# Optimization experiments

Hardware: AMD Instinct MI355X
Metric: run time of the kernel (lower is better)

## Reference

```python
import jax, jax.numpy as jnp
import numpy as np

B, L, NB = 8192, 40, 2        # batch, maxlen, behavior features
V, E = 100000, 64             # vocab per table, embed dim per table
NS, ND = 3, 8                 # other sparse feats, dense feats
D = NB * E                    # concatenated behavior embed dim = 128
ALL = D + D + (ND + NS * E)   # info_all dim = 456
NEG_INF = -2.0**32 + 1
BN_EPS = 1e-3                 # keras BatchNormalization default epsilon


def setup_inputs() -> dict:
    key = jax.random.key(0)
    ks = jax.random.split(key, 20)
    inp = {
        "dense_inputs": jax.random.normal(ks[0], (B, ND), jnp.float32),
        "sparse_inputs": jax.random.randint(ks[1], (B, NS), 0, V),
        "seq_inputs": jax.random.randint(ks[2], (B, L, NB), 0, V),
        "item_inputs": jax.random.randint(ks[3], (B, NB), 0, V),
        # embedding tables (random_uniform init in keras)
        "emb_sparse": jax.random.uniform(ks[4], (NS, V, E), jnp.float32, -0.05, 0.05),
        "emb_seq": jax.random.uniform(ks[5], (NB, V, E), jnp.float32, -0.05, 0.05),
        # attention MLP: input 4*D=512 -> 80 -> 40 -> 1
        "att_W1": jax.random.normal(ks[6], (4 * D, 80), jnp.float32) * 0.05,
        "att_b1": jnp.zeros((80,), jnp.float32),
        "att_W2": jax.random.normal(ks[7], (80, 40), jnp.float32) * 0.05,
        "att_b2": jnp.zeros((40,), jnp.float32),
        "att_Wf": jax.random.normal(ks[8], (40, 1), jnp.float32) * 0.05,
        "att_bf": jnp.zeros((1,), jnp.float32),
        # batch norm (inference-mode moving stats)
        "bn_gamma": jnp.ones((ALL,), jnp.float32),
        "bn_beta": jnp.zeros((ALL,), jnp.float32),
        "bn_mean": jnp.zeros((ALL,), jnp.float32),
        "bn_var": jnp.ones((ALL,), jnp.float32),
        # FFN: ALL -> 80 -> 40 -> 1, PReLU alphas per-feature
        "ffn_W1": jax.random.normal(ks[9], (ALL, 80), jnp.float32) * 0.05,
        "ffn_b1": jnp.zeros((80,), jnp.float32),
        "ffn_a1": jnp.full((80,), 0.25, jnp.float32),
        "ffn_W2": jax.random.normal(ks[10], (80, 40), jnp.float32) * 0.05,
        "ffn_b2": jnp.zeros((40,), jnp.float32),
        "ffn_a2": jnp.full((40,), 0.25, jnp.float32),
        "out_W": jax.random.normal(ks[11], (40, 1), jnp.float32) * 0.05,
        "out_b": jnp.zeros((1,), jnp.float32),
    }
    return inp


def prelu(x, alpha):
    return jnp.where(x > 0, x, alpha * x)


def reference(dense_inputs, sparse_inputs, seq_inputs, item_inputs,
              emb_sparse, emb_seq,
              att_W1, att_b1, att_W2, att_b2, att_Wf, att_bf,
              bn_gamma, bn_beta, bn_mean, bn_var,
              ffn_W1, ffn_b1, ffn_a1, ffn_W2, ffn_b2, ffn_a2,
              out_W, out_b):
    mask = (seq_inputs[:, :, 0] != 0)                                   # [B, L]
    # other sparse embeddings + dense features
    other_info = jnp.concatenate(
        [dense_inputs] + [emb_sparse[i][sparse_inputs[:, i]] for i in range(NS)], axis=-1)
    # behavior sequence / candidate item embeddings
    seq_embed = jnp.concatenate([emb_seq[i][seq_inputs[:, :, i]] for i in range(NB)], axis=-1)  # [B,L,D]
    item_embed = jnp.concatenate([emb_seq[i][item_inputs[:, i]] for i in range(NB)], axis=-1)   # [B,D]

    # local activation attention
    q = jnp.broadcast_to(item_embed[:, None, :], seq_embed.shape)       # [B,L,D]
    info = jnp.concatenate([q, seq_embed, q - seq_embed, q * seq_embed], axis=-1)  # [B,L,4D]
    h = jax.nn.sigmoid(info @ att_W1 + att_b1)
    h = jax.nn.sigmoid(h @ att_W2 + att_b2)
    logits = (h @ att_Wf + att_bf)[..., 0]                               # [B,L]
    logits = jnp.where(mask, logits, NEG_INF)
    att = jax.nn.softmax(logits, axis=-1)                                # [B,L]
    user_info = jnp.einsum('bl,bld->bd', att, seq_embed)                 # [B,D]

    info_all = jnp.concatenate([user_info, item_embed, other_info], axis=-1)  # [B,ALL]
    info_all = bn_gamma * (info_all - bn_mean) * jax.lax.rsqrt(bn_var + BN_EPS) + bn_beta
    info_all = prelu(info_all @ ffn_W1 + ffn_b1, ffn_a1)
    info_all = prelu(info_all @ ffn_W2 + ffn_b2, ffn_a2)
    return jax.nn.sigmoid(info_all @ out_W + out_b)                      # [B,1]
```

## Files before the change

### kernel.cpp

```cpp
#include <hip/hip_runtime.h>

#define BB 8192
#define LL 40
#define VV 100000
#define NEG_INF_F (-4294967295.0f)
#define XS 264
#define HS 104
#define XGS 480

typedef __attribute__((ext_vector_type(8))) short short8;
typedef __attribute__((ext_vector_type(4))) float f32x4;

__device__ __forceinline__ unsigned short f2bf(float f) {
  unsigned u = __float_as_uint(f);
  u += 0x7FFFu + ((u >> 16) & 1u);
  return (unsigned short)(u >> 16);
}
__device__ __forceinline__ float bf2f(unsigned short s) {
  return __uint_as_float(((unsigned)s) << 16);
}

__global__ void prep_all(const float* __restrict__ W1, float* __restrict__ wqcT,
                         unsigned short* __restrict__ WsdpT,
                         const float* __restrict__ aW2, unsigned short* __restrict__ W2bT,
                         const float* __restrict__ fW2, unsigned short* __restrict__ W2fT,
                         const float* __restrict__ fW1, const float* __restrict__ g,
                         const float* __restrict__ vr, unsigned short* __restrict__ W1fT,
                         const float* __restrict__ fb1, const float* __restrict__ be,
                         const float* __restrict__ mn, float* __restrict__ b1p) {
  __shared__ float red[4];
  int bid = blockIdx.x, t = threadIdx.x;
  if (bid < 40) {
    int i = bid * 256 + t;
    int h = i >> 7, k = i & 127;
    float a = W1[k * 80 + h];
    float b = W1[(128 + k) * 80 + h];
    float c = W1[(256 + k) * 80 + h];
    float d = W1[(384 + k) * 80 + h];
    wqcT[h * 132 + k] = a + c;
    WsdpT[h * 256 + k] = f2bf(b - c);
    WsdpT[h * 256 + 128 + k] = f2bf(d);
  } else if (bid < 58) {
    int i = (bid - 40) * 256 + t;
    int n = i / 96, k = i % 96;
    W2bT[i] = (n < 40 && k < 80) ? f2bf(aW2[k * 40 + n]) : (unsigned short)0;
  } else if (bid < 76) {
    int i = (bid - 58) * 256 + t;
    int n = i / 96, k = i % 96;
    W2fT[i] = (n < 40 && k < 80) ? f2bf(fW2[k * 40 + n]) : (unsigned short)0;
  } else if (bid < 226) {
    int i = (bid - 76) * 256 + t;
    int n = i / 480, k = i % 480;
    float v = 0.f;
    if (k < 456) v = fW1[k * 80 + n] * g[k] * rsqrtf(vr[k] + 1e-3f);
    W1fT[i] = f2bf(v);
  } else {
    int n = bid - 226;
    float p = 0.f;
    for (int k = t; k < 456; k += 256) {
      float sc = g[k] * rsqrtf(vr[k] + 1e-3f);
      p += (be[k] - mn[k] * sc) * fW1[k * 80 + n];
    }
    for (int off = 32; off; off >>= 1) p += __shfl_xor(p, off, 64);
    if ((t & 63) == 0) red[t >> 6] = p;
    __syncthreads();
    if (t == 0) b1p[n] = fb1[n] + red[0] + red[1] + red[2] + red[3];
  }
}


__launch_bounds__(256, 5)
__global__ void din_att(const float* __restrict__ dense, const int* __restrict__ sparsei,
                        const int* __restrict__ seqi, const int* __restrict__ itemi,
                        const float* __restrict__ embS, const float* __restrict__ embQ,
                        const float* __restrict__ wqcT, const unsigned short* __restrict__ WsdpT,
                        const unsigned short* __restrict__ W2bT,
                        const float* __restrict__ ab1, const float* __restrict__ ab2,
                        const float* __restrict__ aWf, const float* __restrict__ abf,
                        unsigned short* __restrict__ Xg) {
  __shared__ __align__(16) char smem[31392];
  unsigned short* sX  = (unsigned short*)smem;
  unsigned short* sH1 = (unsigned short*)smem + 10560;
  float* sQ     = (float*)(smem + 29440);
  float* sQC    = sQ + 128;
  float* sOther = sQC + 80;
  float* sAtt   = sOther + 200;
  float* sLogit = sAtt + 40;

  const int t = threadIdx.x;
  const int b = blockIdx.x;
  const int wv = t >> 6, ln = t & 63, m16 = ln & 15, quad = ln >> 4;

  short8 Bf[8];
  {
    const unsigned short* br = WsdpT + (size_t)(wv * 16 + m16) * 256 + quad * 8;
#pragma unroll
    for (int kt = 0; kt < 8; kt++) Bf[kt] = *(const short8*)(br + kt * 32);
  }

  if (t < 32) {
    int f = t >> 4, sub = t & 15;
    int idx = itemi[b * 2 + f];
    float4 v = *(const float4*)(embQ + ((size_t)(f * VV + idx)) * 64 + sub * 4);
    *(float4*)(sQ + f * 64 + sub * 4) = v;
  } else if (t < 80) {
    int j = t - 32, f = j >> 4, sub = j & 15;
    int idx = sparsei[b * 3 + f];
    float4 v = *(const float4*)(embS + ((size_t)(f * VV + idx)) * 64 + sub * 4);
    *(float4*)(sOther + 8 + f * 64 + sub * 4) = v;
  } else if (t < 88) {
    sOther[t - 80] = dense[b * 8 + (t - 80)];
  } else if (t < 128) {
    sLogit[t - 88] = 0.f;
  }
  for (int i = t; i < 1280; i += 256) {
    int r = i >> 4, sub = i & 15;
    int l = r >> 1, f = r & 1;
    int idx = seqi[b * 80 + r];
    float4 v = *(const float4*)(embQ + ((size_t)(f * VV + idx)) * 64 + sub * 4);
    ushort4 u;
    u.x = f2bf(v.x); u.y = f2bf(v.y); u.z = f2bf(v.z); u.w = f2bf(v.w);
    *(ushort4*)(sX + l * XS + f * 64 + sub * 4) = u;
  }
  for (int i = t; i < 320; i += 256) {
    int r = i >> 3, c = i & 7;
    ((unsigned*)sH1)[r * 52 + 40 + c] = 0u;
  }
  __syncthreads();

  if (t < 80) {
    float acc = ab1[t];
    const float* wq = wqcT + t * 132;
    for (int k = 0; k < 128; k += 4) {
      float4 w = *(const float4*)(wq + k);
      float4 q = *(const float4*)(sQ + k);
      acc += q.x * w.x + q.y * w.y + q.z * w.z + q.w * w.w;
    }
    sQC[t] = acc;
  } else {
    for (int i = t - 80; i < 2560; i += 176) {
      int l = i >> 6, kp = i & 63;
      unsigned sv = *(const unsigned*)(sX + l * XS + 2 * kp);
      float s0 = bf2f((unsigned short)sv);
      float s1 = bf2f((unsigned short)(sv >> 16));
      float p0 = sQ[2 * kp] * s0, p1 = sQ[2 * kp + 1] * s1;
      *(unsigned*)(sX + l * XS + 128 + 2 * kp) =
          (unsigned)f2bf(p0) | ((unsigned)f2bf(p1) << 16);
    }
  }
  __syncthreads();

  {
    const int h = wv * 16 + m16;
    const float qc = sQC[h];
#pragma unroll
    for (int mt = 0; mt < 3; mt++) {
      f32x4 acc = {0.f, 0.f, 0.f, 0.f};
      const unsigned short* ar = sX + (mt * 16 + m16) * XS + quad * 8;
#pragma unroll
      for (int kt = 0; kt < 8; kt++) {
        short8 a = *(const short8*)(ar + kt * 32);
        acc = __builtin_amdgcn_mfma_f32_16x16x32_bf16(a, Bf[kt], acc, 0, 0, 0);
      }
#pragma unroll
      for (int r = 0; r < 4; r++) {
        int l = mt * 16 + quad * 4 + r;
        if (l < 40) {
          float z = acc[r] + qc;
          sH1[l * HS + h] = f2bf(1.f / (1.f + __expf(-z)));
        }
      }
    }
    if (wv < 3) {
      short8 B4[8];
      const unsigned short* br = WsdpT + (size_t)(64 + m16) * 256 + quad * 8;
#pragma unroll
      for (int kt = 0; kt < 8; kt++) B4[kt] = *(const short8*)(br + kt * 32);
      f32x4 acc = {0.f, 0.f, 0.f, 0.f};
      const unsigned short* ar = sX + (wv * 16 + m16) * XS + quad * 8;
#pragma unroll
      for (int kt = 0; kt < 8; kt++) {
        short8 a = *(const short8*)(ar + kt * 32);
        acc = __builtin_amdgcn_mfma_f32_16x16x32_bf16(a, B4[kt], acc, 0, 0, 0);
      }
      int h4 = 64 + m16;
      float qc4 = sQC[h4];
#pragma unroll
      for (int r = 0; r < 4; r++) {
        int l = wv * 16 + quad * 4 + r;
        if (l < 40) {
          float z = acc[r] + qc4;
          sH1[l * HS + h4] = f2bf(1.f / (1.f + __expf(-z)));
        }
      }
    }
  }
  __syncthreads();

  for (int tile = wv; tile < 9; tile += 4) {
    int mt = tile / 3, nt = tile % 3;
    f32x4 acc = {0.f, 0.f, 0.f, 0.f};
    const unsigned short* ar = sH1 + (mt * 16 + m16) * HS + quad * 8;
    const unsigned short* br = W2bT + (nt * 16 + m16) * 96 + quad * 8;
#pragma unroll
    for (int kt = 0; kt < 3; kt++) {
      short8 a = *(const short8*)(ar + kt * 32);
      short8 bb = *(const short8*)(br + kt * 32);
      acc = __builtin_amdgcn_mfma_f32_16x16x32_bf16(a, bb, acc, 0, 0, 0);
    }
    int j = nt * 16 + m16;
    float b2 = (j < 40) ? ab2[j] : 0.f;
    float wf = (j < 40) ? aWf[j] : 0.f;
    float c[4];
#pragma unroll
    for (int r = 0; r < 4; r++) {
      float h2 = 1.f / (1.f + __expf(-(acc[r] + b2)));
      c[r] = (j < 40) ? h2 * wf : 0.f;
    }
#pragma unroll
    for (int off = 1; off < 16; off <<= 1) {
#pragma unroll
      for (int r = 0; r < 4; r++) c[r] += __shfl_xor(c[r], off, 64);
    }
    if (m16 == 0) {
#pragma unroll
      for (int r = 0; r < 4; r++) {
        int l = mt * 16 + quad * 4 + r;
        if (l < 40) atomicAdd(&sLogit[l], c[r]);
      }
    }
  }
  __syncthreads();

  if (wv == 0) {
    float logit = -3.0e38f;
    if (t < 40) {
      logit = (seqi[b * 80 + 2 * t] != 0) ? (sLogit[t] + abf[0]) : NEG_INF_F;
    }
    float mx = logit;
    for (int off = 32; off; off >>= 1) mx = fmaxf(mx, __shfl_xor(mx, off, 64));
    float ex = (t < 40) ? __expf(logit - mx) : 0.f;
    float sm = ex;
    for (int off = 32; off; off >>= 1) sm += __shfl_xor(sm, off, 64);
    if (t < 40) sAtt[t] = ex / sm;
  } else {
    int j = t - 64;
    unsigned* xr = (unsigned*)(Xg + (size_t)b * XGS);
    if (j < 64) {
      xr[64 + j] = (unsigned)f2bf(sQ[2 * j]) | ((unsigned)f2bf(sQ[2 * j + 1]) << 16);
    } else if (j < 164) {
      int p = j - 64;
      xr[128 + p] = (unsigned)f2bf(sOther[2 * p]) | ((unsigned)f2bf(sOther[2 * p + 1]) << 16);
    } else if (j < 176) {
      xr[228 + (j - 164)] = 0u;
    }
  }
  __syncthreads();

  if (t < 128) {
    float acc = 0.f;
    for (int l = 0; l < 40; l++) acc += sAtt[l] * bf2f(sX[l * XS + t]);
    Xg[(size_t)b * XGS + t] = f2bf(acc);
  }
}


__launch_bounds__(256, 2)
__global__ void din_ffn(const unsigned short* __restrict__ Xg,
                        const unsigned short* __restrict__ W1fT, const float* __restrict__ b1p,
                        const float* __restrict__ fa1,
                        const unsigned short* __restrict__ W2fT, const float* __restrict__ fb2,
                        const float* __restrict__ fa2,
                        const float* __restrict__ oW, const float* __restrict__ ob,
                        float* __restrict__ out) {
  __shared__ __align__(16) unsigned short sXB[16 * 488];
  __shared__ __align__(16) unsigned short sH1B[16 * HS];
  __shared__ float sH2B[16 * 41];
  const int t = threadIdx.x, blk = blockIdx.x;
  const int wv = t >> 6, ln = t & 63, m16 = ln & 15, quad = ln >> 4;

  short8 Bf[15];
  {
    const unsigned short* br = W1fT + (size_t)(wv * 16 + m16) * 480 + quad * 8;
#pragma unroll
    for (int kt = 0; kt < 15; kt++) Bf[kt] = *(const short8*)(br + kt * 32);
  }

  for (int i = t; i < 960; i += 256) {
    int r = i / 60, c = i % 60;
    *(uint4*)(sXB + r * 488 + c * 8) =
        *(const uint4*)(Xg + (size_t)(blk * 16 + r) * XGS + c * 8);
  }
  if (t < 128) {
    int r = t >> 3, c = t & 7;
    ((unsigned*)sH1B)[r * 52 + 40 + c] = 0u;
  }
  __syncthreads();

  {
    int h = wv * 16 + m16;
    f32x4 acc = {0.f, 0.f, 0.f, 0.f};
    const unsigned short* ar = sXB + m16 * 488 + quad * 8;
#pragma unroll
    for (int kt = 0; kt < 15; kt++) {
      short8 a = *(const short8*)(ar + kt * 32);
      acc = __builtin_amdgcn_mfma_f32_16x16x32_bf16(a, Bf[kt], acc, 0, 0, 0);
    }
    float b1v = b1p[h], a1v = fa1[h];
#pragma unroll
    for (int r = 0; r < 4; r++) {
      int l = quad * 4 + r;
      float z = acc[r] + b1v;
      z = z > 0.f ? z : a1v * z;
      sH1B[l * HS + h] = f2bf(z);
    }
    if (wv == 0) {
      short8 B4[15];
      const unsigned short* br = W1fT + (size_t)(64 + m16) * 480 + quad * 8;
#pragma unroll
      for (int kt = 0; kt < 15; kt++) B4[kt] = *(const short8*)(br + kt * 32);
      f32x4 acc4 = {0.f, 0.f, 0.f, 0.f};
#pragma unroll
      for (int kt = 0; kt < 15; kt++) {
        short8 a = *(const short8*)(ar + kt * 32);
        acc4 = __builtin_amdgcn_mfma_f32_16x16x32_bf16(a, B4[kt], acc4, 0, 0, 0);
      }
      int h4 = 64 + m16;
      float b1v4 = b1p[h4], a1v4 = fa1[h4];
#pragma unroll
      for (int r = 0; r < 4; r++) {
        int l = quad * 4 + r;
        float z = acc4[r] + b1v4;
        z = z > 0.f ? z : a1v4 * z;
        sH1B[l * HS + h4] = f2bf(z);
      }
    }
  }
  __syncthreads();

  if (wv < 3) {
    f32x4 acc = {0.f, 0.f, 0.f, 0.f};
    const unsigned short* ar = sH1B + m16 * HS + quad * 8;
    const unsigned short* br = W2fT + (wv * 16 + m16) * 96 + quad * 8;
#pragma unroll
    for (int kt = 0; kt < 3; kt++) {
      short8 a = *(const short8*)(ar + kt * 32);
      short8 bb = *(const short8*)(br + kt * 32);
      acc = __builtin_amdgcn_mfma_f32_16x16x32_bf16(a, bb, acc, 0, 0, 0);
    }
    int j = wv * 16 + m16;
    if (j < 40) {
      float b2 = fb2[j], a2 = fa2[j];
#pragma unroll
      for (int r = 0; r < 4; r++) {
        int l = quad * 4 + r;
        float z = acc[r] + b2;
        sH2B[l * 41 + j] = z > 0.f ? z : a2 * z;
      }
    }
  }
  __syncthreads();

  if (t < 16) {
    float acc = ob[0];
    for (int j = 0; j < 40; j++) acc += sH2B[t * 41 + j] * oW[j];
    out[blk * 16 + t] = 1.f / (1.f + __expf(-acc));
  }
}


extern "C" void kernel_launch(void* const* d_in, const int* in_sizes, int n_in,
                              void* d_out, int out_size, void* d_ws, size_t ws_size,
                              hipStream_t stream) {
  const float* dense  = (const float*)d_in[0];
  const int*   sparsei = (const int*)d_in[1];
  const int*   seqi   = (const int*)d_in[2];
  const int*   itemi  = (const int*)d_in[3];
  const float* embS   = (const float*)d_in[4];
  const float* embQ   = (const float*)d_in[5];
  const float* aW1    = (const float*)d_in[6];
  const float* ab1    = (const float*)d_in[7];
  const float* aW2    = (const float*)d_in[8];
  const float* ab2    = (const float*)d_in[9];
  const float* aWf    = (const float*)d_in[10];
  const float* abf    = (const float*)d_in[11];
  const float* bng    = (const float*)d_in[12];
  const float* bnb    = (const float*)d_in[13];
  const float* bnm    = (const float*)d_in[14];
  const float* bnv    = (const float*)d_in[15];
  const float* fW1    = (const float*)d_in[16];
  const float* fb1    = (const float*)d_in[17];
  const float* fa1    = (const float*)d_in[18];
  const float* fW2    = (const float*)d_in[19];
  const float* fb2    = (const float*)d_in[20];
  const float* fa2    = (const float*)d_in[21];
  const float* oW     = (const float*)d_in[22];
  const float* ob     = (const float*)d_in[23];
  float* out = (float*)d_out;

  float* ws = (float*)d_ws;
  float* wqcT = ws;
  float* b1p  = ws + 10560;
  unsigned short* WsdpT = (unsigned short*)(ws + 10640);
  unsigned short* W2bT  = (unsigned short*)(ws + 20880);
  unsigned short* W2fT  = (unsigned short*)(ws + 23184);
  unsigned short* W1fT  = (unsigned short*)(ws + 25488);
  unsigned short* Xg    = (unsigned short*)(ws + 44688);

  prep_all<<<306, 256, 0, stream>>>(aW1, wqcT, WsdpT, aW2, W2bT, fW2, W2fT,
                                    fW1, bng, bnv, W1fT, fb1, bnb, bnm, b1p);
  din_att<<<BB, 256, 0, stream>>>(dense, sparsei, seqi, itemi, embS, embQ,
                                  wqcT, WsdpT, W2bT, ab1, ab2, aWf, abf, Xg);
  din_ffn<<<512, 256, 0, stream>>>(Xg, W1fT, b1p, fa1, W2fT, fb2, fa2, oW, ob, out);
}
```

Baseline: 328.1 us.

## Fold item-query product into per-block attention weights to halve MFMA K

The per-element q*seq product columns are no longer built in shared memory. Each block instead forms fused B fragments W_sd + q∘W_d in registers, so the first attention layer runs over K=128 instead of 256. This shrinks the sX tile and total LDS, which allows raising launch bounds to 6 blocks per SM. The query-constant dot product is split across 160 threads, and the sequence mask is precomputed during the gather instead of reread from global memory. The fused weights are rounded to bf16 per batch, which slightly changes numerics.

```diff
diff --git a/kernel.cpp b/kernel.cpp
--- a/kernel.cpp
+++ b/kernel.cpp
@@ -4,7 +4,7 @@
 #define LL 40
 #define VV 100000
 #define NEG_INF_F (-4294967295.0f)
-#define XS 264
+#define XS 136
 #define HS 104
 #define XGS 480
 
@@ -18,6 +18,15 @@
 }
 __device__ __forceinline__ float bf2f(unsigned short s) {
   return __uint_as_float(((unsigned)s) << 16);
+}
+
+__device__ __forceinline__ short8 fuseB(short8 wsd, short8 wd, float4 qa, float4 qb) {
+  float qv[8] = {qa.x, qa.y, qa.z, qa.w, qb.x, qb.y, qb.z, qb.w};
+  short8 o;
+#pragma unroll
+  for (int j = 0; j < 8; j++)
+    o[j] = (short)f2bf(bf2f((unsigned short)wsd[j]) + qv[j] * bf2f((unsigned short)wd[j]));
+  return o;
 }
 
 __global__ void prep_all(const float* __restrict__ W1, float* __restrict__ wqcT,
@@ -69,7 +78,7 @@
 }
 
 
-__launch_bounds__(256, 5)
+__launch_bounds__(256, 6)
 __global__ void din_att(const float* __restrict__ dense, const int* __restrict__ sparsei,
                         const int* __restrict__ seqi, const int* __restrict__ itemi,
                         const float* __restrict__ embS, const float* __restrict__ embQ,
@@ -78,24 +87,28 @@
                         const float* __restrict__ ab1, const float* __restrict__ ab2,
                         const float* __restrict__ aWf, const float* __restrict__ abf,
                         unsigned short* __restrict__ Xg) {
-  __shared__ __align__(16) char smem[31392];
+  __shared__ __align__(16) char smem[21632];
   unsigned short* sX  = (unsigned short*)smem;
-  unsigned short* sH1 = (unsigned short*)smem + 10560;
-  float* sQ     = (float*)(smem + 29440);
-  float* sQC    = sQ + 128;
-  float* sOther = sQC + 80;
+  unsigned short* sH1 = (unsigned short*)(smem + 10880);
+  float* sQ     = (float*)(smem + 19200);
+  float* sQCp   = sQ + 128;
+  float* sOther = sQCp + 160;
   float* sAtt   = sOther + 200;
   float* sLogit = sAtt + 40;
+  float* sMask  = sLogit + 40;
 
   const int t = threadIdx.x;
   const int b = blockIdx.x;
   const int wv = t >> 6, ln = t & 63, m16 = ln & 15, quad = ln >> 4;
 
-  short8 Bf[8];
+  short8 wsdF[4], wdF[4];
   {
     const unsigned short* br = WsdpT + (size_t)(wv * 16 + m16) * 256 + quad * 8;
 #pragma unroll
-    for (int kt = 0; kt < 8; kt++) Bf[kt] = *(const short8*)(br + kt * 32);
+    for (int kt = 0; kt < 4; kt++) {
+      wsdF[kt] = *(const short8*)(br + kt * 32);
+      wdF[kt]  = *(const short8*)(br + 128 + kt * 32);
+    }
   }
 
   if (t < 32) {
@@ -121,6 +134,7 @@
     ushort4 u;
     u.x = f2bf(v.x); u.y = f2bf(v.y); u.z = f2bf(v.z); u.w = f2bf(v.w);
     *(ushort4*)(sX + l * XS + f * 64 + sub * 4) = u;
+    if (((r & 1) | sub) == 0) sMask[l] = (idx != 0) ? 0.f : NEG_INF_F;
   }
   for (int i = t; i < 320; i += 256) {
     int r = i >> 3, c = i & 7;
@@ -128,39 +142,52 @@
   }
   __syncthreads();
 
-  if (t < 80) {
-    float acc = ab1[t];
-    const float* wq = wqcT + t * 132;
-    for (int k = 0; k < 128; k += 4) {
+  if (t < 160) {
+    int h = (t < 80) ? t : t - 80;
+    int k0 = (t < 80) ? 0 : 64;
+    float acc = (t < 80) ? ab1[h] : 0.f;
+    const float* wq = wqcT + h * 132 + k0;
+    const float* qq = sQ + k0;
+    for (int k = 0; k < 64; k += 4) {
       float4 w = *(const float4*)(wq + k);
-      float4 q = *(const float4*)(sQ + k);
+      float4 q = *(const float4*)(qq + k);
       acc += q.x * w.x + q.y * w.y + q.z * w.z + q.w * w.w;
     }
-    sQC[t] = acc;
-  } else {
-    for (int i = t - 80; i < 2560; i += 176) {
-      int l = i >> 6, kp = i & 63;
-      unsigned sv = *(const unsigned*)(sX + l * XS + 2 * kp);
-      float s0 = bf2f((unsigned short)sv);
-      float s1 = bf2f((unsigned short)(sv >> 16));
-      float p0 = sQ[2 * kp] * s0, p1 = sQ[2 * kp + 1] * s1;
-      *(unsigned*)(sX + l * XS + 128 + 2 * kp) =
-          (unsigned)f2bf(p0) | ((unsigned)f2bf(p1) << 16);
+    sQCp[t] = acc;
+  }
+  short8 Bp[4], Bp4[4];
+  {
+#pragma unroll
+    for (int kt = 0; kt < 4; kt++) {
+      int k0 = quad * 8 + kt * 32;
+      float4 qa = *(const float4*)(sQ + k0);
+      float4 qb = *(const float4*)(sQ + k0 + 4);
+      Bp[kt] = fuseB(wsdF[kt], wdF[kt], qa, qb);
+    }
+    if (wv < 3) {
+      const unsigned short* br = WsdpT + (size_t)(64 + m16) * 256 + quad * 8;
+#pragma unroll
+      for (int kt = 0; kt < 4; kt++) {
+        short8 w1 = *(const short8*)(br + kt * 32);
+        short8 w2 = *(const short8*)(br + 128 + kt * 32);
+        int k0 = quad * 8 + kt * 32;
+        Bp4[kt] = fuseB(w1, w2, *(const float4*)(sQ + k0), *(const float4*)(sQ + k0 + 4));
+      }
     }
   }
   __syncthreads();
 
   {
     const int h = wv * 16 + m16;
-    const float qc = sQC[h];
+    const float qc = sQCp[h] + sQCp[80 + h];
 #pragma unroll
     for (int mt = 0; mt < 3; mt++) {
       f32x4 acc = {0.f, 0.f, 0.f, 0.f};
       const unsigned short* ar = sX + (mt * 16 + m16) * XS + quad * 8;
 #pragma unroll
-      for (int kt = 0; kt < 8; kt++) {
+      for (int kt = 0; kt < 4; kt++) {
         short8 a = *(const short8*)(ar + kt * 32);
-        acc = __builtin_amdgcn_mfma_f32_16x16x32_bf16(a, Bf[kt], acc, 0, 0, 0);
+        acc = __builtin_amdgcn_mfma_f32_16x16x32_bf16(a, Bp[kt], acc, 0, 0, 0);
       }
 #pragma unroll
       for (int r = 0; r < 4; r++) {
@@ -172,19 +199,15 @@
       }
     }
     if (wv < 3) {
-      short8 B4[8];
-      const unsigned short* br = WsdpT + (size_t)(64 + m16) * 256 + quad * 8;
-#pragma unroll
-      for (int kt = 0; kt < 8; kt++) B4[kt] = *(const short8*)(br + kt * 32);
       f32x4 acc = {0.f, 0.f, 0.f, 0.f};
       const unsigned short* ar = sX + (wv * 16 + m16) * XS + quad * 8;
 #pragma unroll
-      for (int kt = 0; kt < 8; kt++) {
+      for (int kt = 0; kt < 4; kt++) {
         short8 a = *(const short8*)(ar + kt * 32);
-        acc = __builtin_amdgcn_mfma_f32_16x16x32_bf16(a, B4[kt], acc, 0, 0, 0);
+        acc = __builtin_amdgcn_mfma_f32_16x16x32_bf16(a, Bp4[kt], acc, 0, 0, 0);
       }
       int h4 = 64 + m16;
-      float qc4 = sQC[h4];
+      float qc4 = sQCp[h4] + sQCp[80 + h4];
 #pragma unroll
       for (int r = 0; r < 4; r++) {
         int l = wv * 16 + quad * 4 + r;
@@ -234,9 +257,7 @@
 
   if (wv == 0) {
     float logit = -3.0e38f;
-    if (t < 40) {
-      logit = (seqi[b * 80 + 2 * t] != 0) ? (sLogit[t] + abf[0]) : NEG_INF_F;
-    }
+    if (t < 40) logit = sLogit[t] + abf[0] + sMask[t];
     float mx = logit;
     for (int off = 32; off; off >>= 1) mx = fmaxf(mx, __shfl_xor(mx, off, 64));
     float ex = (t < 40) ? __expf(logit - mx) : 0.f;
```

Measured after the change: 391.7 us. +19.4%, slower.
